# Kernel optimization log

Measured on AMD Instinct MI355X. Metric: run time of the kernel, lower is better.

The kernel has to match this reference:

```python
import jax, jax.numpy as jnp
import numpy as np

B, N, K = 4, 1024, 32
C_S, C_Z, C_H, H, PQ, PV = 384, 128, 16, 12, 4, 8
INF, EPS = 1e5, 1e-8
LN_EPS = 1e-5


def _quat_to_rot(q):
    # q: [..., 4] unit quaternions -> [..., 3, 3]
    w, x, y, z = q[..., 0], q[..., 1], q[..., 2], q[..., 3]
    r = jnp.stack([
        1 - 2 * (y * y + z * z), 2 * (x * y - w * z), 2 * (x * z + w * y),
        2 * (x * y + w * z), 1 - 2 * (x * x + z * z), 2 * (y * z - w * x),
        2 * (x * z - w * y), 2 * (y * z + w * x), 1 - 2 * (x * x + y * y),
    ], axis=-1)
    return r.reshape(q.shape[:-1] + (3, 3))


def _layernorm(x, scale, bias):
    m = jnp.mean(x, axis=-1, keepdims=True)
    v = jnp.mean((x - m) ** 2, axis=-1, keepdims=True)
    return (x - m) * jax.lax.rsqrt(v + LN_EPS) * scale + bias


def setup_inputs():
    key = jax.random.key(0)
    ks = jax.random.split(key, 16)
    s = jax.random.normal(ks[0], (B, N, C_S), jnp.float32)
    z = jax.random.normal(ks[1], (B, N, K, C_Z), jnp.float32)
    edge_index = jax.random.randint(ks[2], (B, N, K), 0, N, jnp.int32)
    quat = jax.random.normal(ks[3], (B, N, 4), jnp.float32)
    rot = _quat_to_rot(quat / jnp.linalg.norm(quat, axis=-1, keepdims=True))
    trans = 10.0 * jax.random.normal(ks[4], (B, N, 3), jnp.float32)
    s_mask = jnp.ones((B, N), jnp.float32)
    sc_s, sc_z = C_S ** -0.5, C_Z ** -0.5
    return {
        "s": s, "z": z, "edge_index": edge_index, "rot": rot, "trans": trans,
        "s_mask": s_mask,
        "ln_s_scale": jnp.ones((C_S,), jnp.float32),
        "ln_s_bias": jnp.zeros((C_S,), jnp.float32),
        "ln_z_scale": jnp.ones((C_Z,), jnp.float32),
        "ln_z_bias": jnp.zeros((C_Z,), jnp.float32),
        "w_q": sc_s * jax.random.normal(ks[5], (C_S, H * C_H), jnp.float32),
        "w_k": sc_s * jax.random.normal(ks[6], (C_S, H * C_H), jnp.float32),
        "w_v": sc_s * jax.random.normal(ks[7], (C_S, H * C_H), jnp.float32),
        "w_q_pts": sc_s * jax.random.normal(ks[8], (C_S, H * PQ * 3), jnp.float32),
        "w_kv_pts": sc_s * jax.random.normal(ks[9], (C_S, H * (PQ + PV) * 3), jnp.float32),
        "w_b": sc_z * jax.random.normal(ks[10], (C_Z, H), jnp.float32),
        "w_down_z": sc_z * jax.random.normal(ks[11], (C_Z, C_Z // 4), jnp.float32),
        "head_weights": jnp.full((H,), 0.541324854612918, jnp.float32),  # softplus^-1(1)
        "w_out": (H * 80) ** -0.5 * jax.random.normal(ks[12], (H * (C_Z // 4 + C_H + PV * 4), C_S), jnp.float32),
    }


def reference(s, z, edge_index, rot, trans, s_mask, ln_s_scale, ln_s_bias,
              ln_z_scale, ln_z_bias, w_q, w_k, w_v, w_q_pts, w_kv_pts, w_b,
              w_down_z, head_weights, w_out):
    bidx = jnp.arange(B)[:, None, None]
    s_ln = _layernorm(s, ln_s_scale, ln_s_bias)          # [B,N,C_S]
    z_ln = _layernorm(z, ln_z_scale, ln_z_bias)          # [B,N,K,C_Z]

    q = (s_ln @ w_q).reshape(B, N, H, C_H)
    k = (s_ln @ w_k)[bidx, edge_index].reshape(B, N, K, H, C_H)
    v = (s_ln @ w_v)[bidx, edge_index].reshape(B, N, K, H, C_H)

    # query points in global frame (query residue's rigid)
    q_pts = (s_ln @ w_q_pts).reshape(B, N, H * PQ, 3)
    q_pts = jnp.einsum('bnij,bnpj->bnpi', rot, q_pts) + trans[:, :, None]
    q_pts = q_pts.reshape(B, N, H, PQ, 3)

    # kv points: gather neighbor local points, then (as in source) apply the
    # QUERY residue's rigid r[..., None, None]
    kv = (s_ln @ w_kv_pts)[bidx, edge_index].reshape(B, N, K, H * (PQ + PV), 3)
    kv = jnp.einsum('bnij,bnkpj->bnkpi', rot, kv) + trans[:, :, None, None]
    kv = kv.reshape(B, N, K, H, PQ + PV, 3)
    k_pts, v_pts = kv[..., :PQ, :], kv[..., PQ:, :]

    b_bias = z_ln @ w_b                                   # [B,N,K,H]
    a = jnp.einsum('bnhc,bnkhc->bnkh', q, k) * (1.0 / (3 * C_H)) ** 0.5
    a = a + (1.0 / 3.0) ** 0.5 * b_bias

    disp = q_pts[:, :, None] - k_pts                      # [B,N,K,H,PQ,3]
    sq = jnp.sum(disp * disp, axis=-1)                    # [B,N,K,H,PQ]
    hw = jax.nn.softplus(head_weights) * (1.0 / (3 * (PQ * 9.0 / 2))) ** 0.5
    a = a - 0.5 * jnp.sum(sq * hw[:, None], axis=-1)      # [B,N,K,H]

    m = s_mask[:, :, None] * s_mask[bidx, edge_index]     # [B,N,K]
    a = a + (INF * (m - 1.0))[..., None]

    a = jax.nn.softmax(jnp.swapaxes(a, -1, -2), axis=-1)  # [B,N,H,K]

    o = jnp.einsum('bnhk,bnkhc->bnhc', a, v).reshape(B, N, H * C_H)

    o_pt = jnp.einsum('bnhk,bnkhvc->bnhvc', a, v_pts)     # [B,N,H,PV,3]
    o_pt = jnp.einsum('bnji,bnhvj->bnhvi', rot, o_pt - trans[:, :, None, None])
    dists = jnp.sqrt(jnp.sum(o_pt * o_pt, axis=-1) + EPS).reshape(B, N, H * PV)
    o_pt_flat = o_pt.reshape(B, N, H * PV * 3)

    o_pair = jnp.einsum('bnhk,bnkc->bnhc', a, z_ln @ w_down_z).reshape(B, N, -1)

    out = jnp.concatenate([o, o_pt_flat, dists, o_pair], axis=-1) @ w_out
    return out
```

## Files before the change

kernel.cpp:

```cpp
#include <hip/hip_runtime.h>
#include <hip/hip_bf16.h>

constexpr int Bb = 4, Nn = 1024, Kk = 32;
constexpr int CS = 384, CZ = 128, CH = 16, Hh = 12, PQn = 4, PVn = 8;
constexpr int NCOLS = 1152;
constexpr int FEAT = 960;
constexpr int NNODE = Bb * Nn;
constexpr int NEDGE = NNODE * Kk;
constexpr int ZOC = 44;
constexpr int NPREP = 1728 + 1440 + 1024 + 1;

constexpr int O_WZP   = 4;
constexpr int O_BVEC  = O_WZP + 6144;
constexpr int O_CSUM  = O_BVEC + 48;
constexpr int O_P     = O_CSUM + 48;
constexpr int O_ZOUT  = O_P + NNODE * NCOLS;
constexpr int O_SLNH  = O_ZOUT + NEDGE * ZOC;
constexpr int O_SLNL  = O_SLNH + NNODE * CS / 2;
constexpr int O_WNTH  = O_SLNL + NNODE * CS / 2;
constexpr int O_WNTL  = O_WNTH + NCOLS * CS / 2;
constexpr int O_WOTH  = O_WNTL + NCOLS * CS / 2;
constexpr int O_WOTL  = O_WOTH + CS * FEAT / 2;
constexpr int O_FEATH = O_SLNH;
constexpr int O_FEATL = O_WOTL + CS * FEAT / 2;
constexpr int TOTAL_F = O_FEATL + NNODE * FEAT / 2;

typedef __attribute__((ext_vector_type(8)))  short short8x;
typedef __attribute__((ext_vector_type(16))) float f32x16;

__device__ __forceinline__ float ldf(const float* p, int i) { return p[i]; }
__device__ __forceinline__ float ldf(const __hip_bfloat16* p, int i) { return __bfloat162float(p[i]); }
__device__ __forceinline__ void stf(float* p, size_t i, float v) { p[i] = v; }
__device__ __forceinline__ void stf(__hip_bfloat16* p, size_t i, float v) { p[i] = __float2bfloat16(v); }
__device__ __forceinline__ float4 ld4(const float* p, size_t i) { return *(const float4*)(p + i); }
__device__ __forceinline__ float4 ld4(const __hip_bfloat16* p, size_t i) {
    ushort4 u = *(const ushort4*)(p + i);
    return make_float4(__uint_as_float((unsigned)u.x << 16),
                       __uint_as_float((unsigned)u.y << 16),
                       __uint_as_float((unsigned)u.z << 16),
                       __uint_as_float((unsigned)u.w << 16));
}
__device__ __forceinline__ void split_bf(float v, unsigned short& h, unsigned short& l) {
    h = (unsigned short)(__float_as_uint(v) >> 16);
    float r = v - __uint_as_float((unsigned)h << 16);
    l = (unsigned short)(__float_as_uint(r) >> 16);
}

__global__ void k_detect(const unsigned* smask_raw, int* flag) {
    if (threadIdx.x == 0) *flag = (smask_raw[0] == 0x3F803F80u) ? 1 : 0;
}

template <typename T>
__global__ __launch_bounds__(256) void k_prep_s(const T* s, const T* lns_sc, const T* lns_bi,
    const T* wq, const T* wk, const T* wv, const T* wqp, const T* wkvp, const T* wout,
    const T* wb, const T* wdz, const T* zsc, const T* zbi, float* wsf,
    const int* flag, int want)
{
    if (flag && *flag != want) return;
    int vb = blockIdx.x, t = threadIdx.x;
    unsigned short* wntH = (unsigned short*)(wsf + O_WNTH);
    unsigned short* wntL = (unsigned short*)(wsf + O_WNTL);
    unsigned short* wotH = (unsigned short*)(wsf + O_WOTH);
    unsigned short* wotL = (unsigned short*)(wsf + O_WOTL);
    unsigned short* slnH = (unsigned short*)(wsf + O_SLNH);
    unsigned short* slnL = (unsigned short*)(wsf + O_SLNL);
    if (vb < 1728) {
        int idx = vb * 256 + t;
        int n = idx / 384, k = idx - n * 384;
        float v;
        if      (n < 192) v = ldf(wq,  k * 192 + n);
        else if (n < 384) v = ldf(wk,  k * 192 + n - 192);
        else if (n < 576) v = ldf(wv,  k * 192 + n - 384);
        else if (n < 720) v = ldf(wqp, k * 144 + n - 576);
        else              v = ldf(wkvp, k * 432 + n - 720);
        unsigned short h, l; split_bf(v, h, l);
        wntH[n * 384 + k] = h; wntL[n * 384 + k] = l;
    } else if (vb < 3168) {
        int idx = (vb - 1728) * 256 + t;
        int n = idx / 960, k = idx - n * 960;
        float v = ldf(wout, k * 384 + n);
        unsigned short h, l; split_bf(v, h, l);
        wotH[n * 960 + k] = h; wotL[n * 960 + k] = l;
    } else if (vb < 4192) {
        int row = (vb - 3168) * 4 + (t >> 6), lane = t & 63;
        float x[6]; float sum = 0, sq = 0;
        #pragma unroll
        for (int j = 0; j < 6; j++) {
            float v = ldf(s, row * CS + lane + 64 * j);
            x[j] = v; sum += v; sq += v * v;
        }
        #pragma unroll
        for (int m = 32; m; m >>= 1) { sum += __shfl_xor(sum, m, 64); sq += __shfl_xor(sq, m, 64); }
        float mean = sum * (1.f / CS);
        float var  = sq * (1.f / CS) - mean * mean;
        float r = rsqrtf(var + 1e-5f);
        #pragma unroll
        for (int j = 0; j < 6; j++) {
            int c = lane + 64 * j;
            float y = (x[j] - mean) * r * ldf(lns_sc, c) + ldf(lns_bi, c);
            unsigned short h, l; split_bf(y, h, l);
            slnH[(size_t)row * CS + c] = h; slnL[(size_t)row * CS + c] = l;
        }
    } else {
        if (t < 128) {
            float sc = ldf(zsc, t);
            for (int o = 0; o < 48; o++) {
                float w = 0.f;
                if (o < 12)      w = ldf(wb, t * 12 + o);
                else if (o < 44) w = ldf(wdz, t * 32 + o - 12);
                wsf[O_WZP + t * 48 + o] = sc * w;
            }
        } else if (t < 176) {
            int o = t - 128;
            float acc = 0.f;
            if (o < 44)
                for (int c = 0; c < 128; c++)
                    acc += ldf(zbi, c) * (o < 12 ? ldf(wb, c * 12 + o) : ldf(wdz, c * 32 + o - 12));
            wsf[O_BVEC + o] = acc;
        } else if (t < 224) {
            int o = t - 176;
            float acc = 0.f;
            if (o < 44)
                for (int c = 0; c < 128; c++)
                    acc += ldf(zsc, c) * (o < 12 ? ldf(wb, c * 12 + o) : ldf(wdz, c * 32 + o - 12));
            wsf[O_CSUM + o] = acc;
        }
    }
}

template <typename T>
__global__ __launch_bounds__(256) void k_zg2(const T* z, const float* wzp, const float* bvec,
                                             const float* csum, float* zout,
                                             const int* flag, int want)
{
    if (flag && *flag != want) return;
    __shared__ float Ws[6144];
    __shared__ float BC[96];
    int t = threadIdx.x;
    for (int i = t; i < 6144; i += 256) Ws[i] = wzp[i];
    if (t < 48) { BC[t] = bvec[t]; BC[48 + t] = csum[t]; }
    __syncthreads();
    size_t e = (size_t)blockIdx.x * 256 + t;
    float4 acc4[11];
    #pragma unroll
    for (int i = 0; i < 11; i++) acc4[i] = make_float4(0.f, 0.f, 0.f, 0.f);
    float sum = 0.f, sq = 0.f;
    for (int c = 0; c < CZ; c += 4) {
        float4 zv = ld4(z, e * CZ + c);
        sum += zv.x + zv.y + zv.z + zv.w;
        sq  += zv.x * zv.x + zv.y * zv.y + zv.z * zv.z + zv.w * zv.w;
        float zz[4] = {zv.x, zv.y, zv.z, zv.w};
        #pragma unroll
        for (int j = 0; j < 4; j++) {
            const float4* wr = (const float4*)&Ws[(c + j) * 48];
            float zc = zz[j];
            #pragma unroll
            for (int i = 0; i < 11; i++) {
                float4 w = wr[i];
                acc4[i].x += zc * w.x; acc4[i].y += zc * w.y;
                acc4[i].z += zc * w.z; acc4[i].w += zc * w.w;
            }
        }
    }
    float mu = sum * (1.f / CZ);
    float rs = rsqrtf(sq * (1.f / CZ) - mu * mu + 1e-5f);
    float* zr = zout + e * ZOC;
    #pragma unroll
    for (int i = 0; i < 11; i++) {
        float4 a = acc4[i];
        float4 bv = *(const float4*)&BC[i * 4];
        float4 cs = *(const float4*)&BC[48 + i * 4];
        float4 o;
        o.x = rs * a.x - rs * mu * cs.x + bv.x;
        o.y = rs * a.y - rs * mu * cs.y + bv.y;
        o.z = rs * a.z - rs * mu * cs.z + bv.z;
        o.w = rs * a.w - rs * mu * cs.w + bv.w;
        *(float4*)(zr + i * 4) = o;
    }
}

#define MFMA3(C, AH, AL, BH, BL)                                              \
    C = __builtin_amdgcn_mfma_f32_32x32x16_bf16(AH, BH, C, 0, 0, 0);          \
    C = __builtin_amdgcn_mfma_f32_32x32x16_bf16(AH, BL, C, 0, 0, 0);          \
    C = __builtin_amdgcn_mfma_f32_32x32x16_bf16(AL, BH, C, 0, 0, 0);

template <typename TO>
__global__ __launch_bounds__(64) void k_mgemm_s(const unsigned short* AH, const unsigned short* AL,
    int lda, const unsigned short* BH, const unsigned short* BL, int ldb,
    TO* C, int ldc, int Kdim, const int* flag, int want)
{
    if (flag && *flag != want) return;
    int bx = blockIdx.x, by = blockIdx.y;
    int l = threadIdx.x, r = l & 31, g = l >> 5;
    size_t a0 = (size_t)(bx * 64 + r) * lda + 8 * g;
    size_t a1 = a0 + (size_t)32 * lda;
    size_t b0 = (size_t)(by * 64 + r) * ldb + 8 * g;
    size_t b1 = b0 + (size_t)32 * ldb;
    f32x16 c00 = {}, c01 = {}, c10 = {}, c11 = {};
    for (int kt = 0; kt < Kdim; kt += 16) {
        short8x aH0 = *(const short8x*)(AH + a0 + kt), aH1 = *(const short8x*)(AH + a1 + kt);
        short8x aL0 = *(const short8x*)(AL + a0 + kt), aL1 = *(const short8x*)(AL + a1 + kt);
        short8x bH0 = *(const short8x*)(BH + b0 + kt), bH1 = *(const short8x*)(BH + b1 + kt);
        short8x bL0 = *(const short8x*)(BL + b0 + kt), bL1 = *(const short8x*)(BL + b1 + kt);
        MFMA3(c00, aH0, aL0, bH0, bL0)
        MFMA3(c01, aH0, aL0, bH1, bL1)
        MFMA3(c10, aH1, aL1, bH0, bL0)
        MFMA3(c11, aH1, aL1, bH1, bL1)
    }
    #pragma unroll
    for (int reg = 0; reg < 16; reg++) {
        int row = (reg & 3) + 8 * (reg >> 2) + 4 * g;
        size_t rm = (size_t)(bx * 64 + row);
        int cn = by * 64 + r;
        stf(C, rm * ldc + cn,             c00[reg]);
        stf(C, rm * ldc + cn + 32,        c01[reg]);
        stf(C, (rm + 32) * ldc + cn,      c10[reg]);
        stf(C, (rm + 32) * ldc + cn + 32, c11[reg]);
    }
}

template <typename T>
__global__ __launch_bounds__(128, 8) void k_attn2(const float* P, const float* zout,
    const int* eidx, const T* smask, const T* rot, const T* hwq,
    unsigned short* featH, unsigned short* featL, const int* flag, int want)
{
    if (flag && *flag != want) return;
    __shared__ float S[1088];
    __shared__ int J[32];
    int bid = blockIdx.x, t = threadIdx.x;
    int node = ((bid & 7) << 9) + (bid >> 3);
    int b = node >> 10;
    const float* Pn = P + (size_t)node * NCOLS;
    for (int u = t; u < 336; u += 128)
        S[u] = (u < 192) ? Pn[u] : Pn[384 + u];
    if (t < 32) {
        int j = eidx[node * Kk + t];
        J[t] = b * Nn + j;
        S[360 + t] = ldf(smask, node) * ldf(smask, b * Nn + j);
    } else if (t < 44) {
        int h = t - 32;
        float x = ldf(hwq, h);
        S[336 + h] = logf(1.f + expf(x)) * 0.13608276348795434f;
    } else if (t < 53) {
        int u = t - 44;
        int i = u / 3, jj = u - i * 3;
        float m = 0;
        #pragma unroll
        for (int l2 = 0; l2 < 3; l2++)
            m += ldf(rot, node * 9 + l2 * 3 + i) * ldf(rot, node * 9 + l2 * 3 + jj);
        S[348 + u] = m;
    }
    __syncthreads();
    #pragma unroll
    for (int it = 0; it < 3; it++) {
        int u = t + 128 * it;
        int h = u >> 5, k = u & 31;
        const float* Pj = P + (size_t)J[k] * NCOLS;
        float qk = 0;
        const float4* pk4 = (const float4*)(Pj + 192 + h * 16);
        const float4* qs4 = (const float4*)(S + h * 16);
        #pragma unroll
        for (int c4 = 0; c4 < 4; c4++) {
            float4 pv = pk4[c4], qv = qs4[c4];
            qk += qv.x * pv.x + qv.y * pv.y + qv.z * pv.z + qv.w * pv.w;
        }
        float M00 = S[348], M01 = S[349], M02 = S[350],
              M11 = S[352], M12 = S[353], M22 = S[356];
        const float4* pp4 = (const float4*)(Pj + 720 + h * 36);
        const float4* qp4 = (const float4*)(S + 192 + h * 12);
        float4 A0 = pp4[0], A1 = pp4[1], A2 = pp4[2];
        float4 B0 = qp4[0], B1 = qp4[1], B2 = qp4[2];
        float d[12] = {B0.x - A0.x, B0.y - A0.y, B0.z - A0.z, B0.w - A0.w,
                       B1.x - A1.x, B1.y - A1.y, B1.z - A1.z, B1.w - A1.w,
                       B2.x - A2.x, B2.y - A2.y, B2.z - A2.z, B2.w - A2.w};
        float sq = 0;
        #pragma unroll
        for (int p = 0; p < 4; p++) {
            float d0 = d[p * 3], d1 = d[p * 3 + 1], d2 = d[p * 3 + 2];
            sq += M00 * d0 * d0 + M11 * d1 * d1 + M22 * d2 * d2
                + 2.f * (M01 * d0 * d1 + M02 * d0 * d2 + M12 * d1 * d2);
        }
        float logit = qk * 0.14433756729740643f
                    + 0.5773502691896258f * zout[((size_t)node * Kk + k) * ZOC + h]
                    - 0.5f * S[336 + h] * sq
                    + 1e5f * (S[360 + k] - 1.f);
        float mx = logit;
        #pragma unroll
        for (int m = 16; m; m >>= 1) mx = fmaxf(mx, __shfl_xor(mx, m, 64));
        float e = expf(logit - mx);
        float ssum = e;
        #pragma unroll
        for (int m = 16; m; m >>= 1) ssum += __shfl_xor(ssum, m, 64);
        S[392 + h * 33 + k] = e / ssum;
    }
    __syncthreads();
    size_t fb = (size_t)node * FEAT;
    for (int u = t; u < 216; u += 128) {
        int h, off, fbase, pair = 0;
        if (u < 48)       { h = u >> 2; off = 384 + h * 16 + (u & 3) * 4; fbase = h * 16 + (u & 3) * 4; }
        else if (u < 120) { int v = u - 48;  h = v / 6; int q = v - h * 6;
                            off = 732 + h * 36 + q * 4; fbase = 192 + h * 24 + q * 4; }
        else              { int v = u - 120; h = v >> 3;
                            off = 12 + (v & 7) * 4; fbase = 576 + h * 32 + (v & 7) * 4; pair = 1; }
        float4 acc = {0.f, 0.f, 0.f, 0.f};
        const float* lrow = S + 392 + h * 33;
        if (!pair) {
            #pragma unroll 8
            for (int k = 0; k < 32; k++) {
                float lw = lrow[k];
                float4 pv = *(const float4*)(P + (size_t)J[k] * NCOLS + off);
                acc.x += lw * pv.x; acc.y += lw * pv.y; acc.z += lw * pv.z; acc.w += lw * pv.w;
            }
        } else {
            const float* zr = zout + (size_t)node * Kk * ZOC + off;
            #pragma unroll 8
            for (int k = 0; k < 32; k++) {
                float lw = lrow[k];
                float4 pv = *(const float4*)(zr + k * ZOC);
                acc.x += lw * pv.x; acc.y += lw * pv.y; acc.z += lw * pv.z; acc.w += lw * pv.w;
            }
        }
        if (u >= 48 && u < 120) {
            *(float4*)&S[788 + (fbase - 192)] = acc;
        } else {
            ushort4 hi, lo;
            split_bf(acc.x, hi.x, lo.x); split_bf(acc.y, hi.y, lo.y);
            split_bf(acc.z, hi.z, lo.z); split_bf(acc.w, hi.w, lo.w);
            *(ushort4*)(featH + fb + fbase) = hi;
            *(ushort4*)(featL + fb + fbase) = lo;
        }
    }
    __syncthreads();
    if (t < 96) {
        float r0 = S[788 + t * 3 + 0];
        float r1 = S[788 + t * 3 + 1];
        float r2 = S[788 + t * 3 + 2];
        float o0 = S[348] * r0 + S[349] * r1 + S[350] * r2;
        float o1 = S[351] * r0 + S[352] * r1 + S[353] * r2;
        float o2 = S[354] * r0 + S[355] * r1 + S[356] * r2;
        unsigned short h, l;
        split_bf(o0, h, l); featH[fb + 192 + t * 3 + 0] = h; featL[fb + 192 + t * 3 + 0] = l;
        split_bf(o1, h, l); featH[fb + 192 + t * 3 + 1] = h; featL[fb + 192 + t * 3 + 1] = l;
        split_bf(o2, h, l); featH[fb + 192 + t * 3 + 2] = h; featL[fb + 192 + t * 3 + 2] = l;
        float dd = sqrtf(o0 * o0 + o1 * o1 + o2 * o2 + 1e-8f);
        split_bf(dd, h, l); featH[fb + 480 + t] = h; featL[fb + 480 + t] = l;
    }
}

template <typename T, typename TO>
static void run_path(const void* s, const void* z, const int* eidx, const void* rot,
                     const void* smask, const void* lns_sc, const void* lns_bi,
                     const void* wq, const void* wk, const void* wv, const void* wqp,
                     const void* wkvp, const void* wb, const void* wdz, const void* zsc,
                     const void* zbi, const void* hwq, const void* wout,
                     float* wsf, void* dout, const int* fg, int want, hipStream_t stream)
{
    unsigned short* slnH = (unsigned short*)(wsf + O_SLNH);
    unsigned short* slnL = (unsigned short*)(wsf + O_SLNL);
    unsigned short* wntH = (unsigned short*)(wsf + O_WNTH);
    unsigned short* wntL = (unsigned short*)(wsf + O_WNTL);
    unsigned short* wotH = (unsigned short*)(wsf + O_WOTH);
    unsigned short* wotL = (unsigned short*)(wsf + O_WOTL);
    unsigned short* featH = (unsigned short*)(wsf + O_FEATH);
    unsigned short* featL = (unsigned short*)(wsf + O_FEATL);

    k_prep_s<T><<<NPREP, 256, 0, stream>>>((const T*)s, (const T*)lns_sc, (const T*)lns_bi,
        (const T*)wq, (const T*)wk, (const T*)wv, (const T*)wqp, (const T*)wkvp,
        (const T*)wout, (const T*)wb, (const T*)wdz, (const T*)zsc, (const T*)zbi, wsf, fg, want);
    k_zg2<T><<<NEDGE / 256, 256, 0, stream>>>((const T*)z, wsf + O_WZP, wsf + O_BVEC,
        wsf + O_CSUM, wsf + O_ZOUT, fg, want);
    k_mgemm_s<float><<<dim3(64, 18), 64, 0, stream>>>(slnH, slnL, CS, wntH, wntL, CS,
        wsf + O_P, NCOLS, CS, fg, want);
    k_attn2<T><<<NNODE, 128, 0, stream>>>(wsf + O_P, wsf + O_ZOUT, eidx, (const T*)smask,
        (const T*)rot, (const T*)hwq, featH, featL, fg, want);
    k_mgemm_s<TO><<<dim3(64, 6), 64, 0, stream>>>(featH, featL, FEAT, wotH, wotL, FEAT,
        (TO*)dout, CS, FEAT, fg, want);
}

extern "C" void kernel_launch(void* const* d_in, const int* in_sizes, int n_in,
                              void* d_out, int out_size, void* d_ws, size_t ws_size,
                              hipStream_t stream) {
    float* wsf = (float*)d_ws;
    int* flag = (int*)d_ws;
    const void* s = d_in[0];   const void* z = d_in[1];
    const int* eidx = (const int*)d_in[2];
    const void* rot = d_in[3];
    const void* smask = d_in[5];
    const void* lns_sc = d_in[6]; const void* lns_bi = d_in[7];
    const void* lnz_sc = d_in[8]; const void* lnz_bi = d_in[9];
    const void* wq = d_in[10]; const void* wk = d_in[11]; const void* wv = d_in[12];
    const void* wqp = d_in[13]; const void* wkvp = d_in[14];
    const void* wb = d_in[15]; const void* wdz = d_in[16];
    const void* hwq = d_in[17]; const void* wout = d_in[18];

    int mode = -1;
    if (in_sizes) {
        if (in_sizes[0] == NNODE * CS * 4) mode = 0;
        else if (in_sizes[0] == NNODE * CS * 2) mode = 1;
    }

    if (mode == 0) {
        run_path<float, float>(s, z, eidx, rot, smask, lns_sc, lns_bi, wq, wk, wv, wqp, wkvp,
                               wb, wdz, lnz_sc, lnz_bi, hwq, wout, wsf, d_out,
                               nullptr, 0, stream);
    } else if (mode == 1) {
        run_path<__hip_bfloat16, __hip_bfloat16>(s, z, eidx, rot, smask, lns_sc, lns_bi,
                               wq, wk, wv, wqp, wkvp, wb, wdz, lnz_sc, lnz_bi, hwq, wout,
                               wsf, d_out, nullptr, 0, stream);
    } else {
        k_detect<<<1, 64, 0, stream>>>((const unsigned*)smask, flag);
        run_path<float, float>(s, z, eidx, rot, smask, lns_sc, lns_bi, wq, wk, wv, wqp, wkvp,
                               wb, wdz, lnz_sc, lnz_bi, hwq, wout, wsf, d_out,
                               flag, 0, stream);
        run_path<__hip_bfloat16, __hip_bfloat16>(s, z, eidx, rot, smask, lns_sc, lns_bi,
                               wq, wk, wv, wqp, wkvp, wb, wdz, lnz_sc, lnz_bi, hwq, wout,
                               wsf, d_out, flag, 1, stream);
    }
}
```

Measured before the change: 337.0 us.

## Read z weights from global, prefetch MFMA operands, stage edge z rows in LDS

Three separate edits. The z-projection kernel drops its LDS copy of the 6144-float weight matrix and reads the weights straight from global memory, relying on cache broadcast, which removes the staging cost and the barrier. The bf16 split GEMM now loads the next k-tile's operands into registers before issuing the current MFMAs (software prefetch), at the cost of more registers. The attention kernel copies each node's 32x44 zout block into shared memory once and reuses it for both the bias logits and the pair aggregation, which raises LDS use per block and may lower occupancy.

```diff
diff --git a/kernel.cpp b/kernel.cpp
--- a/kernel.cpp
+++ b/kernel.cpp
@@ -134,12 +134,7 @@
                                              const int* flag, int want)
 {
     if (flag && *flag != want) return;
-    __shared__ float Ws[6144];
-    __shared__ float BC[96];
     int t = threadIdx.x;
-    for (int i = t; i < 6144; i += 256) Ws[i] = wzp[i];
-    if (t < 48) { BC[t] = bvec[t]; BC[48 + t] = csum[t]; }
-    __syncthreads();
     size_t e = (size_t)blockIdx.x * 256 + t;
     float4 acc4[11];
     #pragma unroll
@@ -152,7 +147,7 @@
         float zz[4] = {zv.x, zv.y, zv.z, zv.w};
         #pragma unroll
         for (int j = 0; j < 4; j++) {
-            const float4* wr = (const float4*)&Ws[(c + j) * 48];
+            const float4* wr = (const float4*)(wzp + (c + j) * 48);
             float zc = zz[j];
             #pragma unroll
             for (int i = 0; i < 11; i++) {
@@ -168,8 +163,8 @@
     #pragma unroll
     for (int i = 0; i < 11; i++) {
         float4 a = acc4[i];
-        float4 bv = *(const float4*)&BC[i * 4];
-        float4 cs = *(const float4*)&BC[48 + i * 4];
+        float4 bv = *(const float4*)(bvec + i * 4);
+        float4 cs = *(const float4*)(csum + i * 4);
         float4 o;
         o.x = rs * a.x - rs * mu * cs.x + bv.x;
         o.y = rs * a.y - rs * mu * cs.y + bv.y;
@@ -197,15 +192,22 @@
     size_t b0 = (size_t)(by * 64 + r) * ldb + 8 * g;
     size_t b1 = b0 + (size_t)32 * ldb;
     f32x16 c00 = {}, c01 = {}, c10 = {}, c11 = {};
+    short8x aH0 = *(const short8x*)(AH + a0), aH1 = *(const short8x*)(AH + a1);
+    short8x aL0 = *(const short8x*)(AL + a0), aL1 = *(const short8x*)(AL + a1);
+    short8x bH0 = *(const short8x*)(BH + b0), bH1 = *(const short8x*)(BH + b1);
+    short8x bL0 = *(const short8x*)(BL + b0), bL1 = *(const short8x*)(BL + b1);
     for (int kt = 0; kt < Kdim; kt += 16) {
-        short8x aH0 = *(const short8x*)(AH + a0 + kt), aH1 = *(const short8x*)(AH + a1 + kt);
-        short8x aL0 = *(const short8x*)(AL + a0 + kt), aL1 = *(const short8x*)(AL + a1 + kt);
-        short8x bH0 = *(const short8x*)(BH + b0 + kt), bH1 = *(const short8x*)(BH + b1 + kt);
-        short8x bL0 = *(const short8x*)(BL + b0 + kt), bL1 = *(const short8x*)(BL + b1 + kt);
+        int kn = (kt + 16 < Kdim) ? kt + 16 : 0;
+        short8x nAH0 = *(const short8x*)(AH + a0 + kn), nAH1 = *(const short8x*)(AH + a1 + kn);
+        short8x nAL0 = *(const short8x*)(AL + a0 + kn), nAL1 = *(const short8x*)(AL + a1 + kn);
+        short8x nBH0 = *(const short8x*)(BH + b0 + kn), nBH1 = *(const short8x*)(BH + b1 + kn);
+        short8x nBL0 = *(const short8x*)(BL + b0 + kn), nBL1 = *(const short8x*)(BL + b1 + kn);
         MFMA3(c00, aH0, aL0, bH0, bL0)
         MFMA3(c01, aH0, aL0, bH1, bL1)
         MFMA3(c10, aH1, aL1, bH0, bL0)
         MFMA3(c11, aH1, aL1, bH1, bL1)
+        aH0 = nAH0; aH1 = nAH1; aL0 = nAL0; aL1 = nAL1;
+        bH0 = nBH0; bH1 = nBH1; bL0 = nBL0; bL1 = nBL1;
     }
     #pragma unroll
     for (int reg = 0; reg < 16; reg++) {
@@ -225,14 +227,20 @@
     unsigned short* featH, unsigned short* featL, const int* flag, int want)
 {
     if (flag && *flag != want) return;
-    __shared__ float S[1088];
+    __shared__ float S[2496];
     __shared__ int J[32];
+    constexpr int ZB = 1088;
     int bid = blockIdx.x, t = threadIdx.x;
     int node = ((bid & 7) << 9) + (bid >> 3);
     int b = node >> 10;
     const float* Pn = P + (size_t)node * NCOLS;
     for (int u = t; u < 336; u += 128)
         S[u] = (u < 192) ? Pn[u] : Pn[384 + u];
+    {
+        const float4* zsrc = (const float4*)(zout + (size_t)node * Kk * ZOC);
+        for (int u = t; u < 352; u += 128)
+            *(float4*)&S[ZB + u * 4] = zsrc[u];
+    }
     if (t < 32) {
         int j = eidx[node * Kk + t];
         J[t] = b * Nn + j;
@@ -281,7 +289,7 @@
                 + 2.f * (M01 * d0 * d1 + M02 * d0 * d2 + M12 * d1 * d2);
         }
         float logit = qk * 0.14433756729740643f
-                    + 0.5773502691896258f * zout[((size_t)node * Kk + k) * ZOC + h]
+                    + 0.5773502691896258f * S[ZB + k * 44 + h]
                     - 0.5f * S[336 + h] * sq
                     + 1e5f * (S[360 + k] - 1.f);
         float mx = logit;
@@ -312,11 +320,10 @@
                 acc.x += lw * pv.x; acc.y += lw * pv.y; acc.z += lw * pv.z; acc.w += lw * pv.w;
             }
         } else {
-            const float* zr = zout + (size_t)node * Kk * ZOC + off;
             #pragma unroll 8
             for (int k = 0; k < 32; k++) {
                 float lw = lrow[k];
-                float4 pv = *(const float4*)(zr + k * ZOC);
+                float4 pv = *(const float4*)&S[ZB + k * 44 + off];
                 acc.x += lw * pv.x; acc.y += lw * pv.y; acc.z += lw * pv.z; acc.w += lw * pv.w;
             }
         }
```

Result: no change. 337.6 us (+0.2%).
